# Kernel optimization log

Measured on AMD Instinct MI355X. Metric: run time of the kernel, lower is better.

## Reference

```python
import jax, jax.numpy as jnp
import numpy as np

N_NODES = 100000
D_FEAT = 128
N_EDGES = 1600000
N_CLASSES = 32


def setup_inputs() -> dict:
    key = jax.random.key(0)
    k1, k2, k3, k4 = jax.random.split(key, 4)
    x = jax.random.normal(k1, (N_NODES, D_FEAT), dtype=jnp.float32)
    edge_index = jax.random.randint(k2, (2, N_EDGES), 0, N_NODES, dtype=jnp.int64)
    # Linear(input_feat, classes) params (PyTorch default init scale)
    bound = 1.0 / np.sqrt(D_FEAT)
    W = jax.random.uniform(k3, (N_CLASSES, D_FEAT), minval=-bound, maxval=bound, dtype=jnp.float32)
    b = jax.random.uniform(k4, (N_CLASSES,), minval=-bound, maxval=bound, dtype=jnp.float32)
    return {"x": x, "edge_index": edge_index, "W": W, "b": b}


def reference(x, edge_index, W, b):
    # GINConv: out = mlp((1 + eps) * x + sum_{j in N(i)} x_j), eps = 0 (default)
    src, dst = edge_index[0], edge_index[1]
    # gather source features [E, D] and scatter-add into target nodes [N, D]
    agg = jax.ops.segment_sum(x[src], dst, num_segments=N_NODES)
    h = x + agg  # (1 + eps) * x with eps = 0
    # Linear: [N, D] @ [D, C] + [C]
    return h @ W.T + b
```

## Files before the change

### kernel.cpp

```cpp
#include <hip/hip_runtime.h>

#define N_NODES 100000
#define D_FEAT 128
#define N_CLASSES 32
#define BSHIFT 8
#define NB 391
#define EPB 4096
#define CAPB 5120
#define GCAP 1536

typedef __attribute__((ext_vector_type(8))) short short8;
typedef __attribute__((ext_vector_type(4))) float f32x4;

__device__ __forceinline__ unsigned short f2bf(float f) {
  unsigned u = __float_as_uint(f);
  u += 0x7fffu + ((u >> 16) & 1);
  return (unsigned short)(u >> 16);
}

__device__ __forceinline__ unsigned cvtpk(float lo, float hi) {
  unsigned r;
  asm("v_cvt_pk_bf16_f32 %0, %1, %2" : "=v"(r) : "v"(lo), "v"(hi));
  return r;
}

__global__ __launch_bounds__(256) void gin_prep(const float* __restrict__ W,
                                                unsigned short* __restrict__ Wb,
                                                int* __restrict__ gcount) {
  int i = blockIdx.x * 256 + threadIdx.x;
  if (i < D_FEAT * N_CLASSES) Wb[i] = f2bf(W[i]);
  if (i < NB) gcount[i] = 0;
}

__global__ __launch_bounds__(256) void gin_mid(
    const float* __restrict__ x, const unsigned short* __restrict__ Wb,
    float* __restrict__ y,
    const int* __restrict__ src, const int* __restrict__ dst,
    int* __restrict__ gcount, unsigned* __restrict__ bucketed,
    int E, int GBr) {
  __shared__ int cnt[NB];
  __shared__ int cur[NB];
  __shared__ int gbase[NB];
  int tid = threadIdx.x;

  if ((int)blockIdx.x >= GBr) {
    int pb = blockIdx.x - GBr;
    int wave = tid >> 6, lane = tid & 63;
    int node_base = pb * 64 + wave * 16;
    if (node_base >= N_NODES) return;
    int m = lane & 15, quad = lane >> 4;

    short8 bfrag[2][4];
#pragma unroll
    for (int cb = 0; cb < 2; ++cb) {
      const unsigned short* wr = Wb + (cb * 16 + m) * D_FEAT + quad * 8;
#pragma unroll
      for (int ks = 0; ks < 4; ++ks)
        bfrag[cb][ks] = *(const short8*)(wr + ks * 32);
    }

    const float* xr = x + (size_t)(node_base + m) * D_FEAT + quad * 8;
    short8 afrag[4];
#pragma unroll
    for (int ks = 0; ks < 4; ++ks) {
      float4 f0 = *(const float4*)(xr + ks * 32);
      float4 f1 = *(const float4*)(xr + ks * 32 + 4);
      union { uint4 u; short8 s; } au;
      au.u.x = cvtpk(f0.x, f0.y);
      au.u.y = cvtpk(f0.z, f0.w);
      au.u.z = cvtpk(f1.x, f1.y);
      au.u.w = cvtpk(f1.z, f1.w);
      afrag[ks] = au.s;
    }

    f32x4 acc0 = {0.f, 0.f, 0.f, 0.f};
    f32x4 acc1 = {0.f, 0.f, 0.f, 0.f};
#pragma unroll
    for (int ks = 0; ks < 4; ++ks) {
      acc0 = __builtin_amdgcn_mfma_f32_16x16x32_bf16(afrag[ks], bfrag[0][ks], acc0, 0, 0, 0);
      acc1 = __builtin_amdgcn_mfma_f32_16x16x32_bf16(afrag[ks], bfrag[1][ks], acc1, 0, 0, 0);
    }

#pragma unroll
    for (int r = 0; r < 4; ++r) {
      int node = node_base + quad * 4 + r;
      y[(size_t)node * N_CLASSES + m] = acc0[r];
      y[(size_t)node * N_CLASSES + 16 + m] = acc1[r];
    }
    return;
  }

  int blk = blockIdx.x;
  for (int i = tid; i < NB; i += 256) {
    cnt[i] = 0;
    cur[i] = 0;
  }
  __syncthreads();
  int base = blk * EPB;
  bool full = (base + EPB <= E);

  int dv[16];
  unsigned sv[16];
  if (full) {
#pragma unroll
    for (int k = 0; k < 16; ++k) dv[k] = dst[base + k * 256 + tid];
#pragma unroll
    for (int k = 0; k < 16; ++k) sv[k] = (unsigned)src[base + k * 256 + tid];
  } else {
#pragma unroll
    for (int k = 0; k < 16; ++k) {
      int e = base + k * 256 + tid;
      dv[k] = (e < E) ? dst[e] : -1;
      sv[k] = (e < E) ? (unsigned)src[e] : 0u;
    }
  }
#pragma unroll
  for (int k = 0; k < 16; ++k)
    if (dv[k] >= 0) atomicAdd(&cnt[dv[k] >> BSHIFT], 1);
  __syncthreads();

  for (int i = tid; i < NB; i += 256) {
    int c = cnt[i];
    gbase[i] = c ? atomicAdd(&gcount[i], c) : 0;
  }
  __syncthreads();

#pragma unroll
  for (int k = 0; k < 16; ++k) {
    if (dv[k] >= 0) {
      int b = dv[k] >> BSHIFT;
      int r = atomicAdd(&cur[b], 1);
      int ga = gbase[b] + r;
      if (ga < CAPB)
        bucketed[(size_t)b * CAPB + ga] = sv[k] | ((unsigned)(dv[k] & 255) << 17);
    }
  }
}

__global__ __launch_bounds__(512) void gin_gather_s(
    const int* __restrict__ gcount, const unsigned* __restrict__ bucketed,
    const float* __restrict__ y, const float* __restrict__ bias,
    float* __restrict__ out) {
  __shared__ unsigned stage[CAPB];
  __shared__ unsigned sorted[GCAP];
  __shared__ int cnt[64];
  __shared__ int off[65];
  __shared__ int cur[64];
  int tid = threadIdx.x;
  int bk = blockIdx.x >> 2;
  int qq = blockIdx.x & 3;
  int len = gcount[bk];
  if (len > CAPB) len = CAPB;
  const unsigned* bb = bucketed + (size_t)bk * CAPB;
  if (tid < 64) cnt[tid] = 0;
  __syncthreads();
  for (int i = tid; i < len; i += 512) {
    unsigned p = bb[i];
    stage[i] = p;
    int n8 = (int)((p >> 17) & 255u);
    if ((n8 >> 6) == qq) atomicAdd(&cnt[n8 & 63], 1);
  }
  __syncthreads();
  if (tid == 0) off[0] = 0;
  if (tid < 64) off[tid + 1] = cnt[tid];
  __syncthreads();
  for (int o = 1; o < 64; o <<= 1) {
    int v = (tid < 64 && tid >= o) ? off[tid + 1 - o] : 0;
    __syncthreads();
    if (tid < 64) off[tid + 1] += v;
    __syncthreads();
  }
  if (tid < 64) cur[tid] = off[tid];
  __syncthreads();
  for (int i = tid; i < len; i += 512) {
    unsigned p = stage[i];
    int n8 = (int)((p >> 17) & 255u);
    if ((n8 >> 6) == qq) {
      int pos = atomicAdd(&cur[n8 & 63], 1);
      if (pos < GCAP) sorted[pos] = p;
    }
  }
  __syncthreads();
  int nl = tid >> 3;
  int q = tid & 7;
  int es = off[nl], ee = off[nl + 1];
  if (ee > GCAP) ee = GCAP;
  if (es > ee) es = ee;
  int node = (bk << 8) + (qq << 6) + nl;
  if (node >= N_NODES) return;
  const float4* y4 = (const float4*)y;
  float4 bq = ((const float4*)bias)[q];
  float4 self = y4[(size_t)node * 8 + q];
  float4 acc;
  acc.x = self.x + bq.x;
  acc.y = self.y + bq.y;
  acc.z = self.z + bq.z;
  acc.w = self.w + bq.w;
  int j = es;
  for (; j + 4 <= ee; j += 4) {
    unsigned s0 = sorted[j] & 0x1FFFF, s1 = sorted[j + 1] & 0x1FFFF;
    unsigned s2 = sorted[j + 2] & 0x1FFFF, s3 = sorted[j + 3] & 0x1FFFF;
    float4 w0 = y4[(size_t)s0 * 8 + q];
    float4 w1 = y4[(size_t)s1 * 8 + q];
    float4 w2 = y4[(size_t)s2 * 8 + q];
    float4 w3 = y4[(size_t)s3 * 8 + q];
    acc.x += w0.x + w1.x + w2.x + w3.x;
    acc.y += w0.y + w1.y + w2.y + w3.y;
    acc.z += w0.z + w1.z + w2.z + w3.z;
    acc.w += w0.w + w1.w + w2.w + w3.w;
  }
  for (; j < ee; ++j) {
    float4 w = y4[(size_t)(sorted[j] & 0x1FFFF) * 8 + q];
    acc.x += w.x; acc.y += w.y; acc.z += w.z; acc.w += w.w;
  }
  ((float4*)out)[(size_t)node * 8 + q] = acc;
}

__global__ __launch_bounds__(256) void gin_bias_init(
    const float* __restrict__ y, const float* __restrict__ b,
    float* __restrict__ out) {
  int gid = blockIdx.x * 256 + threadIdx.x;
  if (gid < N_NODES * N_CLASSES) out[gid] = y[gid] + b[gid & 31];
}
__global__ __launch_bounds__(256) void gin_scatter_fb(
    const int* __restrict__ src, const int* __restrict__ dst,
    const float* __restrict__ y, float* __restrict__ out, int n_edges) {
  long long gid = (long long)blockIdx.x * 256 + threadIdx.x;
  int e = (int)(gid >> 5);
  int c = (int)(gid & 31);
  if (e >= n_edges) return;
  atomicAdd(&out[(size_t)dst[e] * N_CLASSES + c],
            y[(size_t)src[e] * N_CLASSES + c]);
}

extern "C" void kernel_launch(void* const* d_in, const int* in_sizes, int n_in,
                              void* d_out, int out_size, void* d_ws, size_t ws_size,
                              hipStream_t stream) {
  const float* x = (const float*)d_in[0];
  const int* edge_index = (const int*)d_in[1];
  const float* W = (const float*)d_in[2];
  const float* b = (const float*)d_in[3];
  float* out = (float*)d_out;

  int E = in_sizes[1] / 2;
  const int* src = edge_index;
  const int* dst = edge_index + E;

  int GBr = (E + EPB - 1) / EPB;
  int pblocks = (N_NODES + 63) / 64;

  char* ws = (char*)d_ws;
  size_t sz_y = (size_t)N_NODES * N_CLASSES * 4;
  size_t sz_wb = (D_FEAT * N_CLASSES * 2 + 15) & ~15ull;
  size_t sz_bucketed = (((size_t)NB * CAPB * 4) + 15) & ~15ull;
  size_t sz_gcnt = ((size_t)NB * 4 + 15) & ~15ull;

  float* y = (float*)ws;
  unsigned short* Wb = (unsigned short*)(ws + sz_y);
  unsigned* bucketed = (unsigned*)(ws + sz_y + sz_wb);
  int* gcount = (int*)(ws + sz_y + sz_wb + sz_bucketed);
  size_t need = sz_y + sz_wb + sz_bucketed + sz_gcnt;

  bool dense = E > 1750000;

  if (ws_size < need || dense) {
    gin_prep<<<16, 256, 0, stream>>>(W, Wb, (int*)ws);
    gin_mid<<<pblocks, 256, 0, stream>>>(x, Wb, y, src, dst, (int*)ws, (unsigned*)ws, E, 0);
    gin_bias_init<<<(N_NODES * N_CLASSES + 255) / 256, 256, 0, stream>>>(y, b, out);
    long long t2 = (long long)E * N_CLASSES;
    gin_scatter_fb<<<(int)((t2 + 255) / 256), 256, 0, stream>>>(src, dst, y, out, E);
    return;
  }

  gin_prep<<<16, 256, 0, stream>>>(W, Wb, gcount);
  gin_mid<<<GBr + pblocks, 256, 0, stream>>>(x, Wb, y, src, dst, gcount, bucketed, E, GBr);
  gin_gather_s<<<NB * 4, 512, 0, stream>>>(gcount, bucketed, y, b, out);
}
```

Measured before the change: 153.0 us.

## Bucket edges per 64-node group and gather neighbor rows from bf16 copy

Edge bucketing now uses 64-node buckets instead of 256-node buckets with a quarter-split gather. Each gather block reads only its own bucket, so the four blocks per bucket no longer stage and filter the same edges. The projection kernel also writes a bf16 copy of y, and neighbor rows are gathered from it, halving gather bytes. This adds bf16 rounding error to the neighbor sum and an extra y write. The binning blocks now handle 16384 edges each and read dst twice instead of holding edges in registers, which gives fewer, longer blocks.

```diff
diff --git a/kernel.cpp b/kernel.cpp
--- a/kernel.cpp
+++ b/kernel.cpp
@@ -3,11 +3,10 @@
 #define N_NODES 100000
 #define D_FEAT 128
 #define N_CLASSES 32
-#define BSHIFT 8
-#define NB 391
-#define EPB 4096
-#define CAPB 5120
-#define GCAP 1536
+#define B4SHIFT 6
+#define NB4 1563
+#define EPB 16384
+#define CAPB4 1280
 
 typedef __attribute__((ext_vector_type(8))) short short8;
 typedef __attribute__((ext_vector_type(4))) float f32x4;
@@ -29,18 +28,17 @@
                                                 int* __restrict__ gcount) {
   int i = blockIdx.x * 256 + threadIdx.x;
   if (i < D_FEAT * N_CLASSES) Wb[i] = f2bf(W[i]);
-  if (i < NB) gcount[i] = 0;
+  if (i < NB4) gcount[i] = 0;
 }
 
 __global__ __launch_bounds__(256) void gin_mid(
     const float* __restrict__ x, const unsigned short* __restrict__ Wb,
-    float* __restrict__ y,
+    float* __restrict__ y, unsigned short* __restrict__ yh,
     const int* __restrict__ src, const int* __restrict__ dst,
     int* __restrict__ gcount, unsigned* __restrict__ bucketed,
     int E, int GBr) {
-  __shared__ int cnt[NB];
-  __shared__ int cur[NB];
-  __shared__ int gbase[NB];
+  __shared__ int cnt[NB4];
+  __shared__ int gbase[NB4];
   int tid = threadIdx.x;
 
   if ((int)blockIdx.x >= GBr) {
@@ -86,79 +84,66 @@
       int node = node_base + quad * 4 + r;
       y[(size_t)node * N_CLASSES + m] = acc0[r];
       y[(size_t)node * N_CLASSES + 16 + m] = acc1[r];
+      unsigned pk = cvtpk(acc0[r], acc1[r]);
+      yh[(size_t)node * N_CLASSES + m] = (unsigned short)(pk & 0xFFFFu);
+      yh[(size_t)node * N_CLASSES + 16 + m] = (unsigned short)(pk >> 16);
     }
     return;
   }
 
   int blk = blockIdx.x;
-  for (int i = tid; i < NB; i += 256) {
-    cnt[i] = 0;
-    cur[i] = 0;
-  }
+  for (int i = tid; i < NB4; i += 256) cnt[i] = 0;
   __syncthreads();
   int base = blk * EPB;
-  bool full = (base + EPB <= E);
-
-  int dv[16];
-  unsigned sv[16];
-  if (full) {
-#pragma unroll
-    for (int k = 0; k < 16; ++k) dv[k] = dst[base + k * 256 + tid];
-#pragma unroll
-    for (int k = 0; k < 16; ++k) sv[k] = (unsigned)src[base + k * 256 + tid];
-  } else {
-#pragma unroll
-    for (int k = 0; k < 16; ++k) {
-      int e = base + k * 256 + tid;
-      dv[k] = (e < E) ? dst[e] : -1;
-      sv[k] = (e < E) ? (unsigned)src[e] : 0u;
-    }
-  }
-#pragma unroll
-  for (int k = 0; k < 16; ++k)
-    if (dv[k] >= 0) atomicAdd(&cnt[dv[k] >> BSHIFT], 1);
-  __syncthreads();
-
-  for (int i = tid; i < NB; i += 256) {
+
+  for (int k = 0; k < EPB / 256; ++k) {
+    int e = base + k * 256 + tid;
+    if (e < E) atomicAdd(&cnt[dst[e] >> B4SHIFT], 1);
+  }
+  __syncthreads();
+
+  for (int i = tid; i < NB4; i += 256) {
     int c = cnt[i];
     gbase[i] = c ? atomicAdd(&gcount[i], c) : 0;
   }
   __syncthreads();
-
-#pragma unroll
-  for (int k = 0; k < 16; ++k) {
-    if (dv[k] >= 0) {
-      int b = dv[k] >> BSHIFT;
-      int r = atomicAdd(&cur[b], 1);
-      int ga = gbase[b] + r;
-      if (ga < CAPB)
-        bucketed[(size_t)b * CAPB + ga] = sv[k] | ((unsigned)(dv[k] & 255) << 17);
+  for (int i = tid; i < NB4; i += 256) cnt[i] = 0;
+  __syncthreads();
+
+  for (int k = 0; k < EPB / 256; ++k) {
+    int e = base + k * 256 + tid;
+    if (e < E) {
+      int d = dst[e];
+      int b4 = d >> B4SHIFT;
+      int r = atomicAdd(&cnt[b4], 1);
+      int ga = gbase[b4] + r;
+      if (ga < CAPB4)
+        bucketed[(size_t)b4 * CAPB4 + ga] =
+            (unsigned)src[e] | ((unsigned)(d & 63) << 17);
     }
   }
 }
 
 __global__ __launch_bounds__(512) void gin_gather_s(
     const int* __restrict__ gcount, const unsigned* __restrict__ bucketed,
-    const float* __restrict__ y, const float* __restrict__ bias,
-    float* __restrict__ out) {
-  __shared__ unsigned stage[CAPB];
-  __shared__ unsigned sorted[GCAP];
+    const float* __restrict__ y, const unsigned short* __restrict__ yh,
+    const float* __restrict__ bias, float* __restrict__ out) {
+  __shared__ unsigned stage[CAPB4];
+  __shared__ unsigned sorted[CAPB4];
   __shared__ int cnt[64];
   __shared__ int off[65];
   __shared__ int cur[64];
   int tid = threadIdx.x;
-  int bk = blockIdx.x >> 2;
-  int qq = blockIdx.x & 3;
-  int len = gcount[bk];
-  if (len > CAPB) len = CAPB;
-  const unsigned* bb = bucketed + (size_t)bk * CAPB;
+  int b4 = blockIdx.x;
+  int len = gcount[b4];
+  if (len > CAPB4) len = CAPB4;
+  const unsigned* bb = bucketed + (size_t)b4 * CAPB4;
   if (tid < 64) cnt[tid] = 0;
   __syncthreads();
   for (int i = tid; i < len; i += 512) {
     unsigned p = bb[i];
     stage[i] = p;
-    int n8 = (int)((p >> 17) & 255u);
-    if ((n8 >> 6) == qq) atomicAdd(&cnt[n8 & 63], 1);
+    atomicAdd(&cnt[(p >> 17) & 63], 1);
   }
   __syncthreads();
   if (tid == 0) off[0] = 0;
@@ -174,21 +159,17 @@
   __syncthreads();
   for (int i = tid; i < len; i += 512) {
     unsigned p = stage[i];
-    int n8 = (int)((p >> 17) & 255u);
-    if ((n8 >> 6) == qq) {
-      int pos = atomicAdd(&cur[n8 & 63], 1);
-      if (pos < GCAP) sorted[pos] = p;
-    }
+    int pos = atomicAdd(&cur[(p >> 17) & 63], 1);
+    sorted[pos] = p;
   }
   __syncthreads();
   int nl = tid >> 3;
   int q = tid & 7;
   int es = off[nl], ee = off[nl + 1];
-  if (ee > GCAP) ee = GCAP;
-  if (es > ee) es = ee;
-  int node = (bk << 8) + (qq << 6) + nl;
+  int node = (b4 << 6) + nl;
   if (node >= N_NODES) return;
   const float4* y4 = (const float4*)y;
+  const unsigned* yh2 = (const unsigned*)yh;
   float4 bq = ((const float4*)bias)[q];
   float4 self = y4[(size_t)node * 8 + q];
   float4 acc;
@@ -200,18 +181,26 @@
   for (; j + 4 <= ee; j += 4) {
     unsigned s0 = sorted[j] & 0x1FFFF, s1 = sorted[j + 1] & 0x1FFFF;
     unsigned s2 = sorted[j + 2] & 0x1FFFF, s3 = sorted[j + 3] & 0x1FFFF;
-    float4 w0 = y4[(size_t)s0 * 8 + q];
-    float4 w1 = y4[(size_t)s1 * 8 + q];
-    float4 w2 = y4[(size_t)s2 * 8 + q];
-    float4 w3 = y4[(size_t)s3 * 8 + q];
-    acc.x += w0.x + w1.x + w2.x + w3.x;
-    acc.y += w0.y + w1.y + w2.y + w3.y;
-    acc.z += w0.z + w1.z + w2.z + w3.z;
-    acc.w += w0.w + w1.w + w2.w + w3.w;
+    uint2 v0 = *(const uint2*)(yh2 + (size_t)s0 * 16 + q * 2);
+    uint2 v1 = *(const uint2*)(yh2 + (size_t)s1 * 16 + q * 2);
+    uint2 v2 = *(const uint2*)(yh2 + (size_t)s2 * 16 + q * 2);
+    uint2 v3 = *(const uint2*)(yh2 + (size_t)s3 * 16 + q * 2);
+    acc.x += __uint_as_float(v0.x << 16) + __uint_as_float(v1.x << 16) +
+             __uint_as_float(v2.x << 16) + __uint_as_float(v3.x << 16);
+    acc.y += __uint_as_float(v0.x & 0xFFFF0000u) + __uint_as_float(v1.x & 0xFFFF0000u) +
+             __uint_as_float(v2.x & 0xFFFF0000u) + __uint_as_float(v3.x & 0xFFFF0000u);
+    acc.z += __uint_as_float(v0.y << 16) + __uint_as_float(v1.y << 16) +
+             __uint_as_float(v2.y << 16) + __uint_as_float(v3.y << 16);
+    acc.w += __uint_as_float(v0.y & 0xFFFF0000u) + __uint_as_float(v1.y & 0xFFFF0000u) +
+             __uint_as_float(v2.y & 0xFFFF0000u) + __uint_as_float(v3.y & 0xFFFF0000u);
   }
   for (; j < ee; ++j) {
-    float4 w = y4[(size_t)(sorted[j] & 0x1FFFF) * 8 + q];
-    acc.x += w.x; acc.y += w.y; acc.z += w.z; acc.w += w.w;
+    unsigned s = sorted[j] & 0x1FFFF;
+    uint2 v = *(const uint2*)(yh2 + (size_t)s * 16 + q * 2);
+    acc.x += __uint_as_float(v.x << 16);
+    acc.y += __uint_as_float(v.x & 0xFFFF0000u);
+    acc.z += __uint_as_float(v.y << 16);
+    acc.w += __uint_as_float(v.y & 0xFFFF0000u);
   }
   ((float4*)out)[(size_t)node * 8 + q] = acc;
 }
@@ -251,21 +240,24 @@
 
   char* ws = (char*)d_ws;
   size_t sz_y = (size_t)N_NODES * N_CLASSES * 4;
+  size_t sz_yh = (((size_t)N_NODES * N_CLASSES * 2) + 15) & ~15ull;
   size_t sz_wb = (D_FEAT * N_CLASSES * 2 + 15) & ~15ull;
-  size_t sz_bucketed = (((size_t)NB * CAPB * 4) + 15) & ~15ull;
-  size_t sz_gcnt = ((size_t)NB * 4 + 15) & ~15ull;
+  size_t sz_bucketed = (((size_t)NB4 * CAPB4 * 4) + 15) & ~15ull;
+  size_t sz_gcnt = ((size_t)NB4 * 4 + 15) & ~15ull;
 
   float* y = (float*)ws;
-  unsigned short* Wb = (unsigned short*)(ws + sz_y);
-  unsigned* bucketed = (unsigned*)(ws + sz_y + sz_wb);
-  int* gcount = (int*)(ws + sz_y + sz_wb + sz_bucketed);
-  size_t need = sz_y + sz_wb + sz_bucketed + sz_gcnt;
+  unsigned short* yh = (unsigned short*)(ws + sz_y);
+  unsigned short* Wb = (unsigned short*)(ws + sz_y + sz_yh);
+  unsigned* bucketed = (unsigned*)(ws + sz_y + sz_yh + sz_wb);
+  int* gcount = (int*)(ws + sz_y + sz_yh + sz_wb + sz_bucketed);
+  size_t need = sz_y + sz_yh + sz_wb + sz_bucketed + sz_gcnt;
 
   bool dense = E > 1750000;
 
   if (ws_size < need || dense) {
     gin_prep<<<16, 256, 0, stream>>>(W, Wb, (int*)ws);
-    gin_mid<<<pblocks, 256, 0, stream>>>(x, Wb, y, src, dst, (int*)ws, (unsigned*)ws, E, 0);
+    gin_mid<<<pblocks, 256, 0, stream>>>(x, Wb, y, yh, src, dst,
+                                         (int*)ws, (unsigned*)ws, E, 0);
     gin_bias_init<<<(N_NODES * N_CLASSES + 255) / 256, 256, 0, stream>>>(y, b, out);
     long long t2 = (long long)E * N_CLASSES;
     gin_scatter_fb<<<(int)((t2 + 255) / 256), 256, 0, stream>>>(src, dst, y, out, E);
@@ -273,6 +265,7 @@
   }
 
   gin_prep<<<16, 256, 0, stream>>>(W, Wb, gcount);
-  gin_mid<<<GBr + pblocks, 256, 0, stream>>>(x, Wb, y, src, dst, gcount, bucketed, E, GBr);
-  gin_gather_s<<<NB * 4, 512, 0, stream>>>(gcount, bucketed, y, b, out);
-}
+  gin_mid<<<GBr + pblocks, 256, 0, stream>>>(x, Wb, y, yh, src, dst,
+                                             gcount, bucketed, E, GBr);
+  gin_gather_s<<<NB4, 512, 0, stream>>>(gcount, bucketed, y, yh, b, out);
+}
```

New measurement: 197.6 us. +29.2%, slower.

## Fuse partition, projection and gather into one persistent cooperative kernel with bf16 gathers

Applied to the files above, without the earlier changes.

Replaces the three-launch pipeline with a persistent cooperative kernel. Blocks pull partition and projection work units from an atomic queue, meet at a grid-wide sync, then pull gather units. W is now converted to bf16 inside each projection unit, so the separate W prep work goes away. The projection also writes a bf16 copy of y, and the gather reads neighbor rows from it, halving random-access bytes at the cost of reduced accumulation precision. The grid sync and persistent scheduling add overhead, and gather blocks drop from 512 to 256 threads.

```diff
diff --git a/kernel.cpp b/kernel.cpp
--- a/kernel.cpp
+++ b/kernel.cpp
@@ -1,4 +1,7 @@
 #include <hip/hip_runtime.h>
+#include <hip/hip_cooperative_groups.h>
+
+namespace cg = cooperative_groups;
 
 #define N_NODES 100000
 #define D_FEAT 128
@@ -8,97 +11,86 @@
 #define EPB 4096
 #define CAPB 5120
 #define GCAP 1536
+#define PUNITS 1563
+#define NGU (NB * 4)
 
 typedef __attribute__((ext_vector_type(8))) short short8;
 typedef __attribute__((ext_vector_type(4))) float f32x4;
-
-__device__ __forceinline__ unsigned short f2bf(float f) {
-  unsigned u = __float_as_uint(f);
-  u += 0x7fffu + ((u >> 16) & 1);
-  return (unsigned short)(u >> 16);
-}
 
 __device__ __forceinline__ unsigned cvtpk(float lo, float hi) {
   unsigned r;
   asm("v_cvt_pk_bf16_f32 %0, %1, %2" : "=v"(r) : "v"(lo), "v"(hi));
   return r;
 }
-
-__global__ __launch_bounds__(256) void gin_prep(const float* __restrict__ W,
-                                                unsigned short* __restrict__ Wb,
-                                                int* __restrict__ gcount) {
-  int i = blockIdx.x * 256 + threadIdx.x;
-  if (i < D_FEAT * N_CLASSES) Wb[i] = f2bf(W[i]);
-  if (i < NB) gcount[i] = 0;
-}
-
-__global__ __launch_bounds__(256) void gin_mid(
-    const float* __restrict__ x, const unsigned short* __restrict__ Wb,
-    float* __restrict__ y,
+__device__ __forceinline__ float bflo(unsigned v) { return __uint_as_float(v << 16); }
+__device__ __forceinline__ float bfhi(unsigned v) { return __uint_as_float(v & 0xFFFF0000u); }
+
+__device__ __forceinline__ void proj_unit(int pb, int tid,
+    const float* __restrict__ x, const float* __restrict__ W,
+    float* __restrict__ y, unsigned short* __restrict__ yh) {
+  int wave = tid >> 6, lane = tid & 63;
+  int node_base = pb * 64 + wave * 16;
+  if (node_base >= N_NODES) return;
+  int m = lane & 15, quad = lane >> 4;
+
+  short8 bfrag[2][4];
+#pragma unroll
+  for (int cb = 0; cb < 2; ++cb) {
+    const float* wr = W + (cb * 16 + m) * D_FEAT + quad * 8;
+#pragma unroll
+    for (int ks = 0; ks < 4; ++ks) {
+      float4 g0 = *(const float4*)(wr + ks * 32);
+      float4 g1 = *(const float4*)(wr + ks * 32 + 4);
+      union { uint4 u; short8 s; } bu;
+      bu.u.x = cvtpk(g0.x, g0.y);
+      bu.u.y = cvtpk(g0.z, g0.w);
+      bu.u.z = cvtpk(g1.x, g1.y);
+      bu.u.w = cvtpk(g1.z, g1.w);
+      bfrag[cb][ks] = bu.s;
+    }
+  }
+
+  const float* xr = x + (size_t)(node_base + m) * D_FEAT + quad * 8;
+  short8 afrag[4];
+#pragma unroll
+  for (int ks = 0; ks < 4; ++ks) {
+    float4 f0 = *(const float4*)(xr + ks * 32);
+    float4 f1 = *(const float4*)(xr + ks * 32 + 4);
+    union { uint4 u; short8 s; } au;
+    au.u.x = cvtpk(f0.x, f0.y);
+    au.u.y = cvtpk(f0.z, f0.w);
+    au.u.z = cvtpk(f1.x, f1.y);
+    au.u.w = cvtpk(f1.z, f1.w);
+    afrag[ks] = au.s;
+  }
+
+  f32x4 acc0 = {0.f, 0.f, 0.f, 0.f};
+  f32x4 acc1 = {0.f, 0.f, 0.f, 0.f};
+#pragma unroll
+  for (int ks = 0; ks < 4; ++ks) {
+    acc0 = __builtin_amdgcn_mfma_f32_16x16x32_bf16(afrag[ks], bfrag[0][ks], acc0, 0, 0, 0);
+    acc1 = __builtin_amdgcn_mfma_f32_16x16x32_bf16(afrag[ks], bfrag[1][ks], acc1, 0, 0, 0);
+  }
+
+#pragma unroll
+  for (int r = 0; r < 4; ++r) {
+    int node = node_base + quad * 4 + r;
+    y[(size_t)node * N_CLASSES + m] = acc0[r];
+    y[(size_t)node * N_CLASSES + 16 + m] = acc1[r];
+    unsigned pk = cvtpk(acc0[r], acc1[r]);
+    yh[(size_t)node * N_CLASSES + m] = (unsigned short)(pk & 0xFFFFu);
+    yh[(size_t)node * N_CLASSES + 16 + m] = (unsigned short)(pk >> 16);
+  }
+}
+
+__device__ __forceinline__ void partition_unit(int blk, int tid, int E,
     const int* __restrict__ src, const int* __restrict__ dst,
     int* __restrict__ gcount, unsigned* __restrict__ bucketed,
-    int E, int GBr) {
-  __shared__ int cnt[NB];
-  __shared__ int cur[NB];
-  __shared__ int gbase[NB];
-  int tid = threadIdx.x;
-
-  if ((int)blockIdx.x >= GBr) {
-    int pb = blockIdx.x - GBr;
-    int wave = tid >> 6, lane = tid & 63;
-    int node_base = pb * 64 + wave * 16;
-    if (node_base >= N_NODES) return;
-    int m = lane & 15, quad = lane >> 4;
-
-    short8 bfrag[2][4];
-#pragma unroll
-    for (int cb = 0; cb < 2; ++cb) {
-      const unsigned short* wr = Wb + (cb * 16 + m) * D_FEAT + quad * 8;
-#pragma unroll
-      for (int ks = 0; ks < 4; ++ks)
-        bfrag[cb][ks] = *(const short8*)(wr + ks * 32);
-    }
-
-    const float* xr = x + (size_t)(node_base + m) * D_FEAT + quad * 8;
-    short8 afrag[4];
-#pragma unroll
-    for (int ks = 0; ks < 4; ++ks) {
-      float4 f0 = *(const float4*)(xr + ks * 32);
-      float4 f1 = *(const float4*)(xr + ks * 32 + 4);
-      union { uint4 u; short8 s; } au;
-      au.u.x = cvtpk(f0.x, f0.y);
-      au.u.y = cvtpk(f0.z, f0.w);
-      au.u.z = cvtpk(f1.x, f1.y);
-      au.u.w = cvtpk(f1.z, f1.w);
-      afrag[ks] = au.s;
-    }
-
-    f32x4 acc0 = {0.f, 0.f, 0.f, 0.f};
-    f32x4 acc1 = {0.f, 0.f, 0.f, 0.f};
-#pragma unroll
-    for (int ks = 0; ks < 4; ++ks) {
-      acc0 = __builtin_amdgcn_mfma_f32_16x16x32_bf16(afrag[ks], bfrag[0][ks], acc0, 0, 0, 0);
-      acc1 = __builtin_amdgcn_mfma_f32_16x16x32_bf16(afrag[ks], bfrag[1][ks], acc1, 0, 0, 0);
-    }
-
-#pragma unroll
-    for (int r = 0; r < 4; ++r) {
-      int node = node_base + quad * 4 + r;
-      y[(size_t)node * N_CLASSES + m] = acc0[r];
-      y[(size_t)node * N_CLASSES + 16 + m] = acc1[r];
-    }
-    return;
-  }
-
-  int blk = blockIdx.x;
-  for (int i = tid; i < NB; i += 256) {
-    cnt[i] = 0;
-    cur[i] = 0;
-  }
+    int* cnt, int* cur, int* gbase) {
+  for (int i = tid; i < NB; i += 256) { cnt[i] = 0; cur[i] = 0; }
   __syncthreads();
   int base = blk * EPB;
   bool full = (base + EPB <= E);
-
   int dv[16];
   unsigned sv[16];
   if (full) {
@@ -118,13 +110,11 @@
   for (int k = 0; k < 16; ++k)
     if (dv[k] >= 0) atomicAdd(&cnt[dv[k] >> BSHIFT], 1);
   __syncthreads();
-
   for (int i = tid; i < NB; i += 256) {
     int c = cnt[i];
     gbase[i] = c ? atomicAdd(&gcount[i], c) : 0;
   }
   __syncthreads();
-
 #pragma unroll
   for (int k = 0; k < 16; ++k) {
     if (dv[k] >= 0) {
@@ -137,24 +127,18 @@
   }
 }
 
-__global__ __launch_bounds__(512) void gin_gather_s(
+__device__ __forceinline__ void gather_unit(int gu, int tid,
     const int* __restrict__ gcount, const unsigned* __restrict__ bucketed,
-    const float* __restrict__ y, const float* __restrict__ bias,
-    float* __restrict__ out) {
-  __shared__ unsigned stage[CAPB];
-  __shared__ unsigned sorted[GCAP];
-  __shared__ int cnt[64];
-  __shared__ int off[65];
-  __shared__ int cur[64];
-  int tid = threadIdx.x;
-  int bk = blockIdx.x >> 2;
-  int qq = blockIdx.x & 3;
+    const float* __restrict__ y, const unsigned short* __restrict__ yh,
+    const float* __restrict__ bias, float* __restrict__ out,
+    unsigned* stage, unsigned* sorted, int* cnt, int* off, int* cur) {
+  int bk = gu >> 2, qq = gu & 3;
   int len = gcount[bk];
   if (len > CAPB) len = CAPB;
   const unsigned* bb = bucketed + (size_t)bk * CAPB;
   if (tid < 64) cnt[tid] = 0;
   __syncthreads();
-  for (int i = tid; i < len; i += 512) {
+  for (int i = tid; i < len; i += 256) {
     unsigned p = bb[i];
     stage[i] = p;
     int n8 = (int)((p >> 17) & 255u);
@@ -172,7 +156,7 @@
   }
   if (tid < 64) cur[tid] = off[tid];
   __syncthreads();
-  for (int i = tid; i < len; i += 512) {
+  for (int i = tid; i < len; i += 256) {
     unsigned p = stage[i];
     int n8 = (int)((p >> 17) & 255u);
     if ((n8 >> 6) == qq) {
@@ -181,39 +165,127 @@
     }
   }
   __syncthreads();
-  int nl = tid >> 3;
-  int q = tid & 7;
+  int nl = tid >> 2, q4 = tid & 3;
   int es = off[nl], ee = off[nl + 1];
   if (ee > GCAP) ee = GCAP;
   if (es > ee) es = ee;
   int node = (bk << 8) + (qq << 6) + nl;
   if (node >= N_NODES) return;
+  const uint4* yh4 = (const uint4*)yh;
   const float4* y4 = (const float4*)y;
-  float4 bq = ((const float4*)bias)[q];
-  float4 self = y4[(size_t)node * 8 + q];
-  float4 acc;
-  acc.x = self.x + bq.x;
-  acc.y = self.y + bq.y;
-  acc.z = self.z + bq.z;
-  acc.w = self.w + bq.w;
+  float4 sA = y4[(size_t)node * 8 + q4 * 2];
+  float4 sB = y4[(size_t)node * 8 + q4 * 2 + 1];
+  float4 bA = ((const float4*)bias)[q4 * 2];
+  float4 bB = ((const float4*)bias)[q4 * 2 + 1];
+  float4 accA = {sA.x + bA.x, sA.y + bA.y, sA.z + bA.z, sA.w + bA.w};
+  float4 accB = {sB.x + bB.x, sB.y + bB.y, sB.z + bB.z, sB.w + bB.w};
   int j = es;
-  for (; j + 4 <= ee; j += 4) {
+  for (; j + 2 <= ee; j += 2) {
     unsigned s0 = sorted[j] & 0x1FFFF, s1 = sorted[j + 1] & 0x1FFFF;
-    unsigned s2 = sorted[j + 2] & 0x1FFFF, s3 = sorted[j + 3] & 0x1FFFF;
-    float4 w0 = y4[(size_t)s0 * 8 + q];
-    float4 w1 = y4[(size_t)s1 * 8 + q];
-    float4 w2 = y4[(size_t)s2 * 8 + q];
-    float4 w3 = y4[(size_t)s3 * 8 + q];
-    acc.x += w0.x + w1.x + w2.x + w3.x;
-    acc.y += w0.y + w1.y + w2.y + w3.y;
-    acc.z += w0.z + w1.z + w2.z + w3.z;
-    acc.w += w0.w + w1.w + w2.w + w3.w;
-  }
-  for (; j < ee; ++j) {
-    float4 w = y4[(size_t)(sorted[j] & 0x1FFFF) * 8 + q];
-    acc.x += w.x; acc.y += w.y; acc.z += w.z; acc.w += w.w;
-  }
-  ((float4*)out)[(size_t)node * 8 + q] = acc;
+    uint4 v0 = yh4[(size_t)s0 * 4 + q4];
+    uint4 v1 = yh4[(size_t)s1 * 4 + q4];
+    accA.x += bflo(v0.x) + bflo(v1.x);
+    accA.y += bfhi(v0.x) + bfhi(v1.x);
+    accA.z += bflo(v0.y) + bflo(v1.y);
+    accA.w += bfhi(v0.y) + bfhi(v1.y);
+    accB.x += bflo(v0.z) + bflo(v1.z);
+    accB.y += bfhi(v0.z) + bfhi(v1.z);
+    accB.z += bflo(v0.w) + bflo(v1.w);
+    accB.w += bfhi(v0.w) + bfhi(v1.w);
+  }
+  if (j < ee) {
+    unsigned s0 = sorted[j] & 0x1FFFF;
+    uint4 v0 = yh4[(size_t)s0 * 4 + q4];
+    accA.x += bflo(v0.x); accA.y += bfhi(v0.x);
+    accA.z += bflo(v0.y); accA.w += bfhi(v0.y);
+    accB.x += bflo(v0.z); accB.y += bfhi(v0.z);
+    accB.z += bflo(v0.w); accB.w += bfhi(v0.w);
+  }
+  ((float4*)out)[(size_t)node * 8 + q4 * 2] = accA;
+  ((float4*)out)[(size_t)node * 8 + q4 * 2 + 1] = accB;
+}
+
+__global__ __launch_bounds__(256) void gin_prep(int* __restrict__ gcount,
+                                                int* __restrict__ wc) {
+  int i = blockIdx.x * 256 + threadIdx.x;
+  if (i < NB) gcount[i] = 0;
+  if (i < 2) wc[i] = 0;
+}
+
+__global__ void __launch_bounds__(256) gin_coop(
+    const float* __restrict__ x, const float* __restrict__ W,
+    float* __restrict__ y, unsigned short* __restrict__ yh,
+    const int* __restrict__ src, const int* __restrict__ dst,
+    int* __restrict__ gcount, unsigned* __restrict__ bucketed,
+    const float* __restrict__ bias, float* __restrict__ out,
+    int* __restrict__ wc, int E, int GBr) {
+  __shared__ __align__(16) char shraw[27648];
+  __shared__ int s_unit;
+  int tid = threadIdx.x;
+  int* p_cnt = (int*)shraw;
+  int* p_cur = p_cnt + NB;
+  int* p_gbase = p_cur + NB;
+  unsigned* g_stage = (unsigned*)shraw;
+  unsigned* g_sorted = g_stage + CAPB;
+  int* g_cnt = (int*)(g_sorted + GCAP);
+  int* g_off = g_cnt + 64;
+  int* g_cur = g_off + 65;
+  int totalA = GBr + PUNITS;
+
+  while (true) {
+    if (tid == 0) s_unit = atomicAdd(&wc[0], 1);
+    __syncthreads();
+    int u = s_unit;
+    __syncthreads();
+    if (u >= totalA) break;
+    if (u < GBr)
+      partition_unit(u, tid, E, src, dst, gcount, bucketed, p_cnt, p_cur, p_gbase);
+    else
+      proj_unit(u - GBr, tid, x, W, y, yh);
+  }
+
+  __threadfence();
+  cg::this_grid().sync();
+  __threadfence();
+
+  while (true) {
+    if (tid == 0) s_unit = atomicAdd(&wc[1], 1);
+    __syncthreads();
+    int gu = s_unit;
+    __syncthreads();
+    if (gu >= NGU) break;
+    gather_unit(gu, tid, gcount, bucketed, y, yh, bias, out,
+                g_stage, g_sorted, g_cnt, g_off, g_cur);
+  }
+}
+
+__global__ void __launch_bounds__(256) gin_mid_classic(
+    const float* __restrict__ x, const float* __restrict__ W,
+    float* __restrict__ y, unsigned short* __restrict__ yh,
+    const int* __restrict__ src, const int* __restrict__ dst,
+    int* __restrict__ gcount, unsigned* __restrict__ bucketed, int E, int GBr) {
+  __shared__ int cnt[NB];
+  __shared__ int cur[NB];
+  __shared__ int gbase[NB];
+  int tid = threadIdx.x;
+  if ((int)blockIdx.x >= GBr) {
+    proj_unit(blockIdx.x - GBr, tid, x, W, y, yh);
+    return;
+  }
+  partition_unit(blockIdx.x, tid, E, src, dst, gcount, bucketed, cnt, cur, gbase);
+}
+
+__global__ void __launch_bounds__(256) gin_gather_classic(
+    const int* __restrict__ gcount, const unsigned* __restrict__ bucketed,
+    const float* __restrict__ y, const unsigned short* __restrict__ yh,
+    const float* __restrict__ bias, float* __restrict__ out) {
+  __shared__ unsigned stage[CAPB];
+  __shared__ unsigned sorted[GCAP];
+  __shared__ int cnt[64];
+  __shared__ int off[65];
+  __shared__ int cur[64];
+  gather_unit(blockIdx.x, threadIdx.x, gcount, bucketed, y, yh, bias, out,
+              stage, sorted, cnt, off, cur);
 }
 
 __global__ __launch_bounds__(256) void gin_bias_init(
@@ -245,34 +317,54 @@
   int E = in_sizes[1] / 2;
   const int* src = edge_index;
   const int* dst = edge_index + E;
-
   int GBr = (E + EPB - 1) / EPB;
-  int pblocks = (N_NODES + 63) / 64;
 
   char* ws = (char*)d_ws;
   size_t sz_y = (size_t)N_NODES * N_CLASSES * 4;
-  size_t sz_wb = (D_FEAT * N_CLASSES * 2 + 15) & ~15ull;
+  size_t sz_yh = (((size_t)N_NODES * N_CLASSES * 2) + 15) & ~15ull;
   size_t sz_bucketed = (((size_t)NB * CAPB * 4) + 15) & ~15ull;
   size_t sz_gcnt = ((size_t)NB * 4 + 15) & ~15ull;
+  size_t sz_wc = 16;
 
   float* y = (float*)ws;
-  unsigned short* Wb = (unsigned short*)(ws + sz_y);
-  unsigned* bucketed = (unsigned*)(ws + sz_y + sz_wb);
-  int* gcount = (int*)(ws + sz_y + sz_wb + sz_bucketed);
-  size_t need = sz_y + sz_wb + sz_bucketed + sz_gcnt;
+  unsigned short* yh = (unsigned short*)(ws + sz_y);
+  unsigned* bucketed = (unsigned*)(ws + sz_y + sz_yh);
+  int* gcount = (int*)(ws + sz_y + sz_yh + sz_bucketed);
+  int* wc = (int*)(ws + sz_y + sz_yh + sz_bucketed + sz_gcnt);
+  size_t need = sz_y + sz_yh + sz_bucketed + sz_gcnt + sz_wc;
 
   bool dense = E > 1750000;
 
   if (ws_size < need || dense) {
-    gin_prep<<<16, 256, 0, stream>>>(W, Wb, (int*)ws);
-    gin_mid<<<pblocks, 256, 0, stream>>>(x, Wb, y, src, dst, (int*)ws, (unsigned*)ws, E, 0);
+    gin_mid_classic<<<PUNITS, 256, 0, stream>>>(x, W, y, yh, src, dst,
+                                                (int*)ws, (unsigned*)ws, E, 0);
     gin_bias_init<<<(N_NODES * N_CLASSES + 255) / 256, 256, 0, stream>>>(y, b, out);
     long long t2 = (long long)E * N_CLASSES;
     gin_scatter_fb<<<(int)((t2 + 255) / 256), 256, 0, stream>>>(src, dst, y, out, E);
     return;
   }
 
-  gin_prep<<<16, 256, 0, stream>>>(W, Wb, gcount);
-  gin_mid<<<GBr + pblocks, 256, 0, stream>>>(x, Wb, y, src, dst, gcount, bucketed, E, GBr);
-  gin_gather_s<<<NB * 4, 512, 0, stream>>>(gcount, bucketed, y, b, out);
-}
+  gin_prep<<<2, 256, 0, stream>>>(gcount, wc);
+
+  int nbpc = 0;
+  hipError_t oe = hipOccupancyMaxActiveBlocksPerMultiprocessor(&nbpc, gin_coop, 256, 0);
+  bool launched = false;
+  if (oe == hipSuccess && nbpc >= 1) {
+    if (nbpc > 5) nbpc = 5;
+    int grid = nbpc * 256;
+    int maxu = GBr + PUNITS;
+    if (grid > maxu) grid = maxu;
+    void* args[] = {(void*)&x, (void*)&W, (void*)&y, (void*)&yh,
+                    (void*)&src, (void*)&dst, (void*)&gcount, (void*)&bucketed,
+                    (void*)&b, (void*)&out, (void*)&wc, (void*)&E, (void*)&GBr};
+    hipError_t err = hipLaunchCooperativeKernel((const void*)gin_coop,
+                                                dim3(grid), dim3(256),
+                                                args, 0, stream);
+    launched = (err == hipSuccess);
+  }
+  if (!launched) {
+    gin_mid_classic<<<GBr + PUNITS, 256, 0, stream>>>(x, W, y, yh, src, dst,
+                                                      gcount, bucketed, E, GBr);
+    gin_gather_classic<<<NGU, 256, 0, stream>>>(gcount, bucketed, y, yh, b, out);
+  }
+}
```

Result: slower. 344.5 us (+125.2%).
